# Performance work log

Hardware: AMD Instinct MI355X
Metric: run time of the kernel (lower is better)

Reference implementation:

```python
import jax, jax.numpy as jnp
import numpy as np

B, D_IN, D_OUT, M = 4096, 1024, 1024, 16
GAMMA = 2.0


def setup_inputs() -> dict:
    key = jax.random.key(0)
    ks = jax.random.split(key, 5)
    scale_in = 1.0 / np.sqrt(D_IN)
    return {
        "x": jax.random.normal(ks[0], (B, D_IN), dtype=jnp.float32),
        "W": jax.random.normal(ks[1], (M, D_IN, D_OUT), dtype=jnp.float32) * scale_in,
        "b": jax.random.normal(ks[2], (M, D_OUT), dtype=jnp.float32) * 0.01,
        "Wg": jax.random.normal(ks[3], (D_IN, M), dtype=jnp.float32) * scale_in,
        "bg": jax.random.normal(ks[4], (M,), dtype=jnp.float32) * 0.01,
    }


def reference(x, W, b, Wg, bg):
    # Gate: linear -> pow(gamma) -> normalize by row sum -> relu
    gu = x @ Wg + bg                                   # [B, M]
    gp = jnp.power(gu, GAMMA)                          # gamma = 2.0
    gates = jax.nn.relu(gp / jnp.sum(gp, axis=1, keepdims=True))  # [B, M]
    # M dense expert modules: relu(x @ W_m + b_m), gated and summed (AdditionSublayer)
    h = jax.nn.relu(jnp.einsum("bi,mio->bmo", x, W) + b)          # [B, M, D_OUT]
    return jnp.einsum("bm,bmo->bo", gates, h)                     # [B, D_OUT]
```

## Files before the change

### kernel.cpp

```cpp
#include <hip/hip_runtime.h>

typedef unsigned short u16;
typedef __attribute__((ext_vector_type(4))) float f32x4;
typedef __attribute__((ext_vector_type(8))) short bf16x8;
typedef __attribute__((ext_vector_type(4))) unsigned short u16x4;

#define BM 128
#define BN 128
#define BK 64
#define NKT 16
#define EPB 8
#define NSTEP (EPB*NKT)

__device__ __forceinline__ u16 f2bf(float f) {
  union { float f; unsigned u; } v; v.f = f;
  unsigned r = v.u + 0x7FFFu + ((v.u >> 16) & 1u);
  return (u16)(r >> 16);
}

__global__ __launch_bounds__(256) void k_cvt_x(const float* __restrict__ x, u16* __restrict__ xb) {
  int i = blockIdx.x * 256 + threadIdx.x;
  f32x4 v = ((const f32x4*)x)[i];
  u16x4 o;
  o.x = f2bf(v.x); o.y = f2bf(v.y); o.z = f2bf(v.z); o.w = f2bf(v.w);
  ((u16x4*)xb)[i] = o;
}

__global__ __launch_bounds__(256) void k_tw(const float* __restrict__ W, u16* __restrict__ wt) {
  __shared__ float t[64][65];
  int bid = blockIdx.x;
  int e = bid >> 8, rem = bid & 255, kt = rem >> 4, nt = rem & 15;
  int tid = threadIdx.x;
  int c = tid & 63, r0 = tid >> 6;
  const float* src = W + (size_t)e * 1048576 + (size_t)(kt * 64) * 1024 + nt * 64;
  #pragma unroll
  for (int p = 0; p < 16; ++p) {
    int r = r0 + p * 4;
    t[r][c] = src[r * 1024 + c];
  }
  __syncthreads();
  u16* dst = wt + (size_t)e * 1048576 + (size_t)(nt * 64) * 1024 + kt * 64;
  #pragma unroll
  for (int p = 0; p < 16; ++p) {
    int r2 = r0 + p * 4;
    dst[r2 * 1024 + c] = f2bf(t[c][r2]);
  }
}

__global__ __launch_bounds__(256) void k_gates(const float* __restrict__ x, const float* __restrict__ Wg,
                                               const float* __restrict__ bg, float* __restrict__ gates) {
  int wid = threadIdx.x >> 6, lane = threadIdx.x & 63;
  int b = blockIdx.x * 4 + wid;
  const float* xr = x + (size_t)b * 1024;
  float acc[16];
  #pragma unroll
  for (int m = 0; m < 16; ++m) acc[m] = 0.f;
  for (int i = lane; i < 1024; i += 64) {
    float xv = xr[i];
    const f32x4* wg = (const f32x4*)(Wg + (size_t)i * 16);
    #pragma unroll
    for (int q = 0; q < 4; ++q) {
      f32x4 w = wg[q];
      acc[q*4+0] += xv * w.x; acc[q*4+1] += xv * w.y;
      acc[q*4+2] += xv * w.z; acc[q*4+3] += xv * w.w;
    }
  }
  #pragma unroll
  for (int m = 0; m < 16; ++m) {
    #pragma unroll
    for (int off = 32; off > 0; off >>= 1)
      acc[m] += __shfl_xor(acc[m], off, 64);
  }
  float tot = 0.f, gp[16];
  #pragma unroll
  for (int m = 0; m < 16; ++m) { float gu = acc[m] + bg[m]; gp[m] = gu * gu; tot += gp[m]; }
  float inv = 1.f / tot;
  if (lane == 0) {
    #pragma unroll
    for (int m = 0; m < 16; ++m) gates[(size_t)b * 16 + m] = gp[m] * inv;
  }
}

__global__ __launch_bounds__(256, 2)
void k_moe(const u16* __restrict__ xb, const u16* __restrict__ wt,
           const float* __restrict__ gates, const float* __restrict__ bias,
           float* __restrict__ out0, float* __restrict__ out1) {
  __shared__ __align__(16) u16 lsA[2][BM * BK];
  __shared__ __align__(16) u16 lsB[2][BN * BK];
  __shared__ float lgat[16][128];

  int tid = threadIdx.x;
  int bid = blockIdx.x;
  int swz = (bid & 7) * 64 + (bid >> 3);
  int btile = swz & 31;
  int grp = swz >> 5;
  int ntile = grp >> 1;
  int mhalf = grp & 1;
  int brow0 = btile * BM;
  int ncol0 = ntile * BN;
  int mb = mhalf * EPB;

  {
    const float* gsrc = gates + (size_t)brow0 * 16;
    #pragma unroll
    for (int i = 0; i < 8; ++i) {
      int idx = i * 256 + tid;
      lgat[idx & 15][idx >> 4] = gsrc[idx];
    }
  }

  int wid = tid >> 6, lane = tid & 63;
  int wm = wid >> 1, wn = wid & 1;
  int lrow = lane & 15, lk = lane >> 4;
  int sw = lrow & 7;

  f32x4 acc[4][4], oacc[4][4];
  #pragma unroll
  for (int i = 0; i < 4; ++i)
    #pragma unroll
    for (int j = 0; j < 4; ++j) {
      f32x4 z; z.x = 0.f; z.y = 0.f; z.z = 0.f; z.w = 0.f;
      acc[i][j] = z; oacc[i][j] = z;
    }

  const u16* asrc = xb + (size_t)brow0 * 1024;

  auto stage = [&](const u16* src, u16* dst) {
    #pragma unroll
    for (int it = 0; it < 4; ++it) {
      int idx = it * 256 + tid;
      int r = idx >> 3, s = idx & 7;
      int g = s ^ (r & 7);
      const u16* ga = src + (size_t)r * 1024 + g * 8;
      u16* la = dst + (size_t)(it * 256 + wid * 64) * 8;
      __builtin_amdgcn_global_load_lds((const __attribute__((address_space(1))) void*)ga,
                                       (__attribute__((address_space(3))) void*)la, 16, 0, 0);
    }
  };

  int abase = (wm * 64 + lrow) * 64;
  int bbase = (wn * 64 + lrow) * 64;

  stage(asrc, lsA[0]);
  stage(wt + (size_t)mb * 1048576 + (size_t)ncol0 * 1024, lsB[0]);
  __syncthreads();

  int cur = 0;
  for (int s = 0; s < NSTEP; ++s) {
    int ns = s + 1;
    if (ns < NSTEP) {
      int kt = ns & (NKT - 1);
      int me = mb + (ns >> 4);
      stage(asrc + kt * BK, lsA[cur ^ 1]);
      stage(wt + (size_t)me * 1048576 + (size_t)ncol0 * 1024 + kt * BK, lsB[cur ^ 1]);
    }
    #pragma unroll
    for (int ks = 0; ks < 2; ++ks) {
      int kg = ((ks * 4 + lk) ^ sw) * 8;
      bf16x8 af[4], bfr[4];
      #pragma unroll
      for (int i = 0; i < 4; ++i) {
        af[i]  = *(const bf16x8*)&lsA[cur][abase + i * 1024 + kg];
        bfr[i] = *(const bf16x8*)&lsB[cur][bbase + i * 1024 + kg];
      }
      #pragma unroll
      for (int mi = 0; mi < 4; ++mi)
        #pragma unroll
        for (int ni = 0; ni < 4; ++ni)
          acc[mi][ni] = __builtin_amdgcn_mfma_f32_16x16x32_bf16(af[mi], bfr[ni], acc[mi][ni], 0, 0, 0);
    }
    __syncthreads();
    if ((s & (NKT - 1)) == (NKT - 1)) {
      int me = mb + (s >> 4);
      float bv[4];
      #pragma unroll
      for (int ni = 0; ni < 4; ++ni) bv[ni] = bias[(size_t)me * 1024 + ncol0 + wn * 64 + ni * 16 + lrow];
      #pragma unroll
      for (int mi = 0; mi < 4; ++mi) {
        float gv[4];
        #pragma unroll
        for (int j = 0; j < 4; ++j) gv[j] = lgat[me][wm * 64 + mi * 16 + lk * 4 + j];
        #pragma unroll
        for (int ni = 0; ni < 4; ++ni) {
          #pragma unroll
          for (int j = 0; j < 4; ++j) {
            float h = acc[mi][ni][j] + bv[ni];
            h = fmaxf(h, 0.f);
            oacc[mi][ni][j] += gv[j] * h;
          }
          f32x4 z; z.x = 0.f; z.y = 0.f; z.z = 0.f; z.w = 0.f;
          acc[mi][ni] = z;
        }
      }
    }
    cur ^= 1;
  }

  float* op = mhalf ? out1 : out0;
  #pragma unroll
  for (int mi = 0; mi < 4; ++mi)
    #pragma unroll
    for (int j = 0; j < 4; ++j) {
      int row = brow0 + wm * 64 + mi * 16 + lk * 4 + j;
      #pragma unroll
      for (int ni = 0; ni < 4; ++ni) {
        int col = ncol0 + wn * 64 + ni * 16 + lrow;
        op[(size_t)row * 1024 + col] = oacc[mi][ni][j];
      }
    }
}

__global__ __launch_bounds__(256) void k_add(float* __restrict__ out, const float* __restrict__ p1) {
  int i = blockIdx.x * 256 + threadIdx.x;
  f32x4 a = ((const f32x4*)out)[i];
  f32x4 b = ((const f32x4*)p1)[i];
  ((f32x4*)out)[i] = a + b;
}

extern "C" void kernel_launch(void* const* d_in, const int* in_sizes, int n_in,
                              void* d_out, int out_size, void* d_ws, size_t ws_size,
                              hipStream_t stream) {
  const float* x  = (const float*)d_in[0];
  const float* W  = (const float*)d_in[1];
  const float* b  = (const float*)d_in[2];
  const float* Wg = (const float*)d_in[3];
  const float* bg = (const float*)d_in[4];
  float* out = (float*)d_out;

  char* ws = (char*)d_ws;
  u16* xb     = (u16*)ws;
  u16* wt     = (u16*)(ws + 8388608);
  float* gts  = (float*)(ws + 41943040);
  float* p1   = (float*)(ws + 42205184);

  k_cvt_x<<<4096, 256, 0, stream>>>(x, xb);
  k_tw<<<4096, 256, 0, stream>>>(W, wt);
  k_gates<<<1024, 256, 0, stream>>>(x, Wg, bg, gts);
  k_moe<<<512, 256, 0, stream>>>(xb, wt, gts, b, out, p1);
  k_add<<<4096, 256, 0, stream>>>(out, p1);
}
```

Before: 218.8 us.

## Restructure MoE GEMM to 128x256 tiles with 3-stage LDS pipeline

The main kernel now launches 256 blocks of 512 threads, each computing a 128x256 output tile with 8 waves, instead of 512 blocks of 256 threads on 128x128 tiles. It adds a triple-buffered global_load_lds pipeline that prefetches two steps ahead and uses explicit vmcnt waits in place of a full __syncthreads per step. MFMA batches are interleaved with partial LDS loads and prefetches, wrapped in setprio and s_barrier. Bias and gates are staged into LDS up front. The aim is to raise reuse of each loaded tile and hide memory latency better, at the cost of more LDS and fewer blocks, which may reduce occupancy.

```diff
diff --git a/kernel.cpp b/kernel.cpp
--- a/kernel.cpp
+++ b/kernel.cpp
@@ -5,17 +5,16 @@
 typedef __attribute__((ext_vector_type(8))) short bf16x8;
 typedef __attribute__((ext_vector_type(4))) unsigned short u16x4;
 
-#define BM 128
-#define BN 128
-#define BK 64
-#define NKT 16
-#define EPB 8
-#define NSTEP (EPB*NKT)
+#define NT 128
 
 __device__ __forceinline__ u16 f2bf(float f) {
   union { float f; unsigned u; } v; v.f = f;
   unsigned r = v.u + 0x7FFFu + ((v.u >> 16) & 1u);
   return (u16)(r >> 16);
+}
+
+__device__ __forceinline__ f32x4 zero4() {
+  f32x4 z; z.x = 0.f; z.y = 0.f; z.z = 0.f; z.w = 0.f; return z;
 }
 
 __global__ __launch_bounds__(256) void k_cvt_x(const float* __restrict__ x, u16* __restrict__ xb) {
@@ -81,122 +80,177 @@
   }
 }
 
-__global__ __launch_bounds__(256, 2)
+#define GLL(srcaddr, ldsaddr) \
+  __builtin_amdgcn_global_load_lds((const __attribute__((address_space(1))) void*)(srcaddr), \
+                                   (__attribute__((address_space(3))) void*)(ldsaddr), 16, 0, 0)
+
+#define MFMA8(m0) do { \
+  acc[m0][0]   = __builtin_amdgcn_mfma_f32_16x16x32_bf16(af0, bfr0, acc[m0][0], 0,0,0);   \
+  acc[m0][1]   = __builtin_amdgcn_mfma_f32_16x16x32_bf16(af0, bfr1, acc[m0][1], 0,0,0);   \
+  acc[m0][2]   = __builtin_amdgcn_mfma_f32_16x16x32_bf16(af0, bfr2, acc[m0][2], 0,0,0);   \
+  acc[m0][3]   = __builtin_amdgcn_mfma_f32_16x16x32_bf16(af0, bfr3, acc[m0][3], 0,0,0);   \
+  acc[m0+1][0] = __builtin_amdgcn_mfma_f32_16x16x32_bf16(af1, bfr0, acc[m0+1][0], 0,0,0); \
+  acc[m0+1][1] = __builtin_amdgcn_mfma_f32_16x16x32_bf16(af1, bfr1, acc[m0+1][1], 0,0,0); \
+  acc[m0+1][2] = __builtin_amdgcn_mfma_f32_16x16x32_bf16(af1, bfr2, acc[m0+1][2], 0,0,0); \
+  acc[m0+1][3] = __builtin_amdgcn_mfma_f32_16x16x32_bf16(af1, bfr3, acc[m0+1][3], 0,0,0); \
+} while (0)
+
+__global__ __launch_bounds__(512, 2)
 void k_moe(const u16* __restrict__ xb, const u16* __restrict__ wt,
            const float* __restrict__ gates, const float* __restrict__ bias,
-           float* __restrict__ out0, float* __restrict__ out1) {
-  __shared__ __align__(16) u16 lsA[2][BM * BK];
-  __shared__ __align__(16) u16 lsB[2][BN * BK];
-  __shared__ float lgat[16][128];
+           float* __restrict__ out0, float* __restrict__ p1out) {
+  __shared__ __align__(16) u16 sA[3 * 8192];
+  __shared__ __align__(16) u16 sB[3 * 16384];
+  __shared__ float lgat[1024];
+  __shared__ float lbias[2048];
 
   int tid = threadIdx.x;
   int bid = blockIdx.x;
-  int swz = (bid & 7) * 64 + (bid >> 3);
+  int swz = (bid & 7) * 32 + (bid >> 3);
   int btile = swz & 31;
-  int grp = swz >> 5;
-  int ntile = grp >> 1;
-  int mhalf = grp & 1;
-  int brow0 = btile * BM;
-  int ncol0 = ntile * BN;
-  int mb = mhalf * EPB;
-
-  {
-    const float* gsrc = gates + (size_t)brow0 * 16;
-    #pragma unroll
-    for (int i = 0; i < 8; ++i) {
-      int idx = i * 256 + tid;
-      lgat[idx & 15][idx >> 4] = gsrc[idx];
-    }
-  }
+  int pnl = swz >> 5;
+  int grp = pnl >> 2;
+  int ntile = pnl & 3;
+  int brow0 = btile * 128;
+  int ncol0 = ntile * 256;
+  int mb = grp * 8;
 
   int wid = tid >> 6, lane = tid & 63;
-  int wm = wid >> 1, wn = wid & 1;
+  int wm = wid >> 2, wn = wid & 3;
   int lrow = lane & 15, lk = lane >> 4;
   int sw = lrow & 7;
 
+  const u16* asrc = xb + (size_t)brow0 * 1024;
+  const u16* bsrc = wt + (size_t)mb * 1048576 + (size_t)ncol0 * 1024;
+
+  int r0a = tid >> 3, s0a = tid & 7;
+  int r1a = (512 + tid) >> 3, s1a = tid & 7;
+  int sia0 = r0a * 1024 + (s0a ^ (r0a & 7)) * 8;
+  int sia1 = r1a * 1024 + (s1a ^ (r1a & 7)) * 8;
+  int lda0 = (wid * 64) * 8;
+  int lda1 = (512 + wid * 64) * 8;
+  int sib0 = sia0, sib1 = sia1;
+  int r2b = (1024 + tid) >> 3;
+  int r3b = (1536 + tid) >> 3;
+  int sib2 = r2b * 1024 + ((tid & 7) ^ (r2b & 7)) * 8;
+  int sib3 = r3b * 1024 + ((tid & 7) ^ (r3b & 7)) * 8;
+  int ldb0 = lda0, ldb1 = lda1;
+  int ldb2 = (1024 + wid * 64) * 8;
+  int ldb3 = (1536 + wid * 64) * 8;
+
+  int baseA = (wm * 64 + lrow) * 64;
+  int baseB = (wn * 64 + lrow) * 64;
+  int pa0 = baseA + ((0 + lk) ^ sw) * 8;
+  int pa1 = baseA + ((4 + lk) ^ sw) * 8;
+  int pb0 = baseB + ((0 + lk) ^ sw) * 8;
+  int pb1 = baseB + ((4 + lk) ^ sw) * 8;
+
   f32x4 acc[4][4], oacc[4][4];
   #pragma unroll
   for (int i = 0; i < 4; ++i)
     #pragma unroll
-    for (int j = 0; j < 4; ++j) {
-      f32x4 z; z.x = 0.f; z.y = 0.f; z.z = 0.f; z.w = 0.f;
-      acc[i][j] = z; oacc[i][j] = z;
-    }
-
-  const u16* asrc = xb + (size_t)brow0 * 1024;
-
-  auto stage = [&](const u16* src, u16* dst) {
-    #pragma unroll
-    for (int it = 0; it < 4; ++it) {
-      int idx = it * 256 + tid;
-      int r = idx >> 3, s = idx & 7;
-      int g = s ^ (r & 7);
-      const u16* ga = src + (size_t)r * 1024 + g * 8;
-      u16* la = dst + (size_t)(it * 256 + wid * 64) * 8;
-      __builtin_amdgcn_global_load_lds((const __attribute__((address_space(1))) void*)ga,
-                                       (__attribute__((address_space(3))) void*)la, 16, 0, 0);
-    }
-  };
-
-  int abase = (wm * 64 + lrow) * 64;
-  int bbase = (wn * 64 + lrow) * 64;
-
-  stage(asrc, lsA[0]);
-  stage(wt + (size_t)mb * 1048576 + (size_t)ncol0 * 1024, lsB[0]);
+    for (int j = 0; j < 4; ++j) { acc[i][j] = zero4(); oacc[i][j] = zero4(); }
+
+  #pragma unroll
+  for (int i = 0; i < 2; ++i) {
+    int idx = i * 512 + tid;
+    lgat[idx] = gates[(size_t)(brow0 + (idx & 127)) * 16 + mb + (idx >> 7)];
+  }
+  #pragma unroll
+  for (int i = 0; i < 4; ++i) {
+    int idx = i * 512 + tid;
+    lbias[idx] = bias[(size_t)(mb + (idx >> 8)) * 1024 + ncol0 + (idx & 255)];
+  }
+  u16 *a0 = sA, *a1 = sA + 8192, *a2 = sA + 16384;
+  u16 *b0 = sB, *b1 = sB + 16384, *b2 = sB + 32768;
+  GLL(asrc + sia0, a0 + lda0); GLL(asrc + sia1, a0 + lda1);
+  GLL(bsrc + sib0, b0 + ldb0); GLL(bsrc + sib1, b0 + ldb1);
+  GLL(bsrc + sib2, b0 + ldb2); GLL(bsrc + sib3, b0 + ldb3);
+  GLL(asrc + 64 + sia0, a1 + lda0); GLL(asrc + 64 + sia1, a1 + lda1);
+  GLL(bsrc + 64 + sib0, b1 + ldb0); GLL(bsrc + 64 + sib1, b1 + ldb1);
+  GLL(bsrc + 64 + sib2, b1 + ldb2); GLL(bsrc + 64 + sib3, b1 + ldb3);
   __syncthreads();
 
-  int cur = 0;
-  for (int s = 0; s < NSTEP; ++s) {
-    int ns = s + 1;
-    if (ns < NSTEP) {
-      int kt = ns & (NKT - 1);
-      int me = mb + (ns >> 4);
-      stage(asrc + kt * BK, lsA[cur ^ 1]);
-      stage(wt + (size_t)me * 1048576 + (size_t)ncol0 * 1024 + kt * BK, lsB[cur ^ 1]);
-    }
-    #pragma unroll
-    for (int ks = 0; ks < 2; ++ks) {
-      int kg = ((ks * 4 + lk) ^ sw) * 8;
-      bf16x8 af[4], bfr[4];
+  for (int t = 0; t < NT; ++t) {
+    int t2 = t + 2;
+    const u16* sa2 = asrc + (t2 & 15) * 64;
+    const u16* sb2 = bsrc + (size_t)(t2 >> 4) * 1048576 + (t2 & 15) * 64;
+    bool pf = (t2 < NT);
+    bf16x8 bfr0, bfr1, bfr2, bfr3, af0, af1;
+
+    bfr0 = *(const bf16x8*)&b0[pb0];
+    bfr1 = *(const bf16x8*)&b0[pb0 + 1024];
+    bfr2 = *(const bf16x8*)&b0[pb0 + 2048];
+    bfr3 = *(const bf16x8*)&b0[pb0 + 3072];
+    af0 = *(const bf16x8*)&a0[pa0];
+    af1 = *(const bf16x8*)&a0[pa0 + 1024];
+    if (pf) { GLL(sa2 + sia0, a2 + lda0); GLL(sa2 + sia1, a2 + lda1); }
+    __builtin_amdgcn_s_barrier();
+    __builtin_amdgcn_s_setprio(1);
+    MFMA8(0);
+    __builtin_amdgcn_s_setprio(0);
+    __builtin_amdgcn_s_barrier();
+
+    af0 = *(const bf16x8*)&a0[pa0 + 2048];
+    af1 = *(const bf16x8*)&a0[pa0 + 3072];
+    if (pf) { GLL(sb2 + sib0, b2 + ldb0); GLL(sb2 + sib1, b2 + ldb1); }
+    __builtin_amdgcn_s_barrier();
+    __builtin_amdgcn_s_setprio(1);
+    MFMA8(2);
+    __builtin_amdgcn_s_setprio(0);
+    __builtin_amdgcn_s_barrier();
+
+    bfr0 = *(const bf16x8*)&b0[pb1];
+    bfr1 = *(const bf16x8*)&b0[pb1 + 1024];
+    bfr2 = *(const bf16x8*)&b0[pb1 + 2048];
+    bfr3 = *(const bf16x8*)&b0[pb1 + 3072];
+    af0 = *(const bf16x8*)&a0[pa1];
+    af1 = *(const bf16x8*)&a0[pa1 + 1024];
+    if (pf) { GLL(sb2 + sib2, b2 + ldb2); GLL(sb2 + sib3, b2 + ldb3); }
+    __builtin_amdgcn_s_barrier();
+    __builtin_amdgcn_s_setprio(1);
+    MFMA8(0);
+    __builtin_amdgcn_s_setprio(0);
+    __builtin_amdgcn_s_barrier();
+
+    af0 = *(const bf16x8*)&a0[pa1 + 2048];
+    af1 = *(const bf16x8*)&a0[pa1 + 3072];
+    __builtin_amdgcn_s_barrier();
+    __builtin_amdgcn_s_setprio(1);
+    MFMA8(2);
+    __builtin_amdgcn_s_setprio(0);
+
+    if ((t & 15) == 15) {
+      int ml = t >> 4;
+      float bvv[4];
       #pragma unroll
-      for (int i = 0; i < 4; ++i) {
-        af[i]  = *(const bf16x8*)&lsA[cur][abase + i * 1024 + kg];
-        bfr[i] = *(const bf16x8*)&lsB[cur][bbase + i * 1024 + kg];
-      }
-      #pragma unroll
-      for (int mi = 0; mi < 4; ++mi)
-        #pragma unroll
-        for (int ni = 0; ni < 4; ++ni)
-          acc[mi][ni] = __builtin_amdgcn_mfma_f32_16x16x32_bf16(af[mi], bfr[ni], acc[mi][ni], 0, 0, 0);
-    }
-    __syncthreads();
-    if ((s & (NKT - 1)) == (NKT - 1)) {
-      int me = mb + (s >> 4);
-      float bv[4];
-      #pragma unroll
-      for (int ni = 0; ni < 4; ++ni) bv[ni] = bias[(size_t)me * 1024 + ncol0 + wn * 64 + ni * 16 + lrow];
+      for (int ni = 0; ni < 4; ++ni) bvv[ni] = lbias[ml * 256 + wn * 64 + ni * 16 + lrow];
       #pragma unroll
       for (int mi = 0; mi < 4; ++mi) {
-        float gv[4];
-        #pragma unroll
-        for (int j = 0; j < 4; ++j) gv[j] = lgat[me][wm * 64 + mi * 16 + lk * 4 + j];
+        f32x4 gv = *(const f32x4*)&lgat[ml * 128 + wm * 64 + mi * 16 + lk * 4];
         #pragma unroll
         for (int ni = 0; ni < 4; ++ni) {
           #pragma unroll
           for (int j = 0; j < 4; ++j) {
-            float h = acc[mi][ni][j] + bv[ni];
+            float h = acc[mi][ni][j] + bvv[ni];
             h = fmaxf(h, 0.f);
             oacc[mi][ni][j] += gv[j] * h;
           }
-          f32x4 z; z.x = 0.f; z.y = 0.f; z.z = 0.f; z.w = 0.f;
-          acc[mi][ni] = z;
+          acc[mi][ni] = zero4();
         }
       }
     }
-    cur ^= 1;
-  }
-
-  float* op = mhalf ? out1 : out0;
+
+    if (t < NT - 2)       asm volatile("s_waitcnt vmcnt(6)" ::: "memory");
+    else if (t == NT - 2) asm volatile("s_waitcnt vmcnt(0)" ::: "memory");
+    __builtin_amdgcn_s_barrier();
+    __builtin_amdgcn_sched_barrier(0);
+
+    u16* ta = a0; a0 = a1; a1 = a2; a2 = ta;
+    u16* tb = b0; b0 = b1; b1 = b2; b2 = tb;
+  }
+
+  float* op = grp ? p1out : out0;
   #pragma unroll
   for (int mi = 0; mi < 4; ++mi)
     #pragma unroll
@@ -236,6 +290,6 @@
   k_cvt_x<<<4096, 256, 0, stream>>>(x, xb);
   k_tw<<<4096, 256, 0, stream>>>(W, wt);
   k_gates<<<1024, 256, 0, stream>>>(x, Wg, bg, gts);
-  k_moe<<<512, 256, 0, stream>>>(xb, wt, gts, b, out, p1);
+  k_moe<<<256, 512, 0, stream>>>(xb, wt, gts, b, out, p1);
   k_add<<<4096, 256, 0, stream>>>(out, p1);
 }
```

New measurement: 194.1 us. -11.3%, faster.
